# Optimization experiments

Hardware: AMD Instinct MI355X
Metric: run time of the kernel (lower is better)

The kernel has to match this reference:

```python
import jax, jax.numpy as jnp
import numpy as np

MARGIN = 0.2
LAMBDA_CLS = 1.0
LAMBDA_TRIPLET = 1.0
EPS = 1e-6  # matches torch pairwise_distance eps inside TripletMarginLoss
B, D, C = 8192, 192, 1024


def setup_inputs() -> dict:
    key = jax.random.key(0)
    k1, k2, k3 = jax.random.split(key, 3)
    embeddings = jax.random.normal(k1, (B, D), dtype=jnp.float32)
    logits = jax.random.normal(k2, (B, C), dtype=jnp.float32)
    targets = jax.random.randint(k3, (B,), 0, C, dtype=jnp.int64)
    return {"embeddings": embeddings, "logits": logits, "targets": targets}


def reference(embeddings, logits, targets):
    # ---- classification loss: mean cross entropy ----
    logp = jax.nn.log_softmax(logits, axis=-1)
    cls_loss = -jnp.mean(jnp.take_along_axis(logp, targets[:, None], axis=1))

    # ---- vectorized hard triplet mining (mining='hard'), on detached embeddings ----
    e = jax.lax.stop_gradient(embeddings)
    sq = jnp.sum(e * e, axis=1)                       # [B]
    d2 = sq[:, None] + sq[None, :] - 2.0 * (e @ e.T)  # [B, B]
    dist = jnp.sqrt(jnp.maximum(d2, 0.0))

    same = targets[:, None] == targets[None, :]       # [B, B]
    eye = jnp.eye(targets.shape[0], dtype=bool)
    pos_mask = same & ~eye
    neg_mask = ~same
    valid = pos_mask.any(axis=1) & neg_mask.any(axis=1)

    # hard positive: farthest same-speaker; hard negative: closest other-speaker
    pos_idx = jnp.argmax(jnp.where(pos_mask, dist, -jnp.inf), axis=1)
    neg_idx = jnp.argmin(jnp.where(neg_mask, dist, jnp.inf), axis=1)

    # ---- triplet margin loss on live embeddings ----
    a = embeddings
    p = embeddings[pos_idx]
    n = embeddings[neg_idx]
    d_ap = jnp.linalg.norm(a - p + EPS, axis=1)
    d_an = jnp.linalg.norm(a - n + EPS, axis=1)
    per_triplet = jnp.maximum(d_ap - d_an + MARGIN, 0.0)

    w = valid.astype(per_triplet.dtype)
    cnt = jnp.sum(w)
    trip_loss = jnp.where(cnt > 0, jnp.sum(per_triplet * w) / jnp.maximum(cnt, 1.0), 0.0)

    return LAMBDA_CLS * cls_loss + LAMBDA_TRIPLET * trip_loss
```

## Files before the change

### kernel.cpp

```cpp
#include <hip/hip_runtime.h>
#include <math.h>

#define B_N    8192
#define D_DIM  192
#define C_CLS  1024
#define MARGIN 0.2f
#define EPS_T  1e-6f

#define TI     128
#define TJ     128
#define JSPLIT 4
#define JLEN   (B_N / JSPLIT)
#define NT     (JLEN / TJ)
#define RB     384

typedef short v8s  __attribute__((ext_vector_type(8)));
typedef float v16f __attribute__((ext_vector_type(16)));

typedef __attribute__((address_space(3))) unsigned int       lds_u32;
typedef __attribute__((address_space(1))) const unsigned int glb_u32;

__device__ __forceinline__ void gll16(const void* g, void* l) {
  __builtin_amdgcn_global_load_lds((glb_u32*)g, (lds_u32*)l, 16, 0, 0);
}

__device__ __forceinline__ int swzb(int r, int cb) {
  return r * RB + (cb ^ ((r & 7) << 4));
}

__device__ __forceinline__ void stage_tile(char* dst, const char* src, int tid) {
  #pragma unroll
  for (int k = 0; k < 6; ++k) {
    int c  = k * 512 + tid;
    int r  = c / 24;
    int cb = (c - r * 24) * 16;
    gll16(src + r * RB + (cb ^ ((r & 7) << 4)),
          dst + (k * 512 + (tid & ~63)) * 16);
  }
}

__device__ __forceinline__ unsigned fkey(float f) {
  unsigned u = __float_as_uint(f);
  return (u & 0x80000000u) ? ~u : (u | 0x80000000u);
}

__device__ __forceinline__ unsigned short to_bf(float x) {
  unsigned u = __float_as_uint(x);
  u += 0x7fffu + ((u >> 16) & 1u);
  return (unsigned short)(u >> 16);
}

__global__ __launch_bounds__(256) void prep_kernel(
    const float* __restrict__ e, unsigned short* __restrict__ ebf,
    float* __restrict__ sq,
    unsigned long long* __restrict__ posw, unsigned long long* __restrict__ negw,
    float* __restrict__ accum) {
  int w = threadIdx.x >> 6, lane = threadIdx.x & 63;
  int row = blockIdx.x * 4 + w;
  const float* p = e + (size_t)row * D_DIM;
  float v0 = p[lane], v1 = p[lane + 64], v2 = p[lane + 128];
  unsigned short* q = ebf + (size_t)row * D_DIM;
  q[lane] = to_bf(v0); q[lane + 64] = to_bf(v1); q[lane + 128] = to_bf(v2);
  float s = v0 * v0 + v1 * v1 + v2 * v2;
  #pragma unroll
  for (int off = 32; off; off >>= 1) s += __shfl_xor(s, off);
  if (lane == 0) sq[row] = s;
  int b = blockIdx.x;
  if (b < 32)       posw[b * 256 + threadIdx.x] = 0ULL;
  else if (b < 64)  negw[(b - 32) * 256 + threadIdx.x] = ~0ULL;
  else if (b == 64 && threadIdx.x < 4) ((unsigned*)accum)[threadIdx.x] = 0u;
}

__global__ __launch_bounds__(512, 1) void mine_kernel(
    const unsigned short* __restrict__ ebf, const int* __restrict__ tgt,
    const float* __restrict__ sq, const float* __restrict__ logits,
    unsigned long long* __restrict__ posw, unsigned long long* __restrict__ negw,
    float* __restrict__ accum) {
  __shared__ unsigned short buf[2][TJ * (RB / 2)];
  __shared__ int   lds_t[2][TJ];
  __shared__ float lds_s[2][TJ];
  __shared__ unsigned long long pmrg[TI];
  __shared__ unsigned long long nmrg[TI];
  __shared__ float ce_part[8];

  const int tid  = threadIdx.x;
  const int w    = tid >> 6;
  const int lane = tid & 63;
  const int n5   = lane & 31;
  const int h    = lane >> 5;
  const int wj   = w & 3;
  const int wi   = w >> 2;
  const int i0 = blockIdx.x * TI;
  const int jb = blockIdx.y * JLEN;

  char* bufA = (char*)buf[0];
  char* bufB = (char*)buf[1];

  if (tid < TI) { pmrg[tid] = 0ULL; nmrg[tid] = ~0ULL; }

  stage_tile(bufB, (const char*)(ebf + (size_t)i0 * D_DIM), tid);
  stage_tile(bufA, (const char*)(ebf + (size_t)jb * D_DIM), tid);
  if (tid < TJ) { lds_t[0][tid] = tgt[jb + tid]; lds_s[0][tid] = sq[jb + tid]; }
  __syncthreads();

  v8s bfrag[2][12];
  #pragma unroll
  for (int tb = 0; tb < 2; ++tb)
    #pragma unroll
    for (int kc = 0; kc < 12; ++kc)
      bfrag[tb][kc] = *(const v8s*)(bufB + swzb(wi * 64 + tb * 32 + n5, kc * 32 + h * 16));

  int my_t[2];
  #pragma unroll
  for (int tb = 0; tb < 2; ++tb) my_t[tb] = tgt[i0 + wi * 64 + tb * 32 + n5];

  __syncthreads();

  float    pv[2] = {-3.4e38f, -3.4e38f}, nv[2] = {3.4e38f, 3.4e38f};
  unsigned pi_[2] = {0u, 0u}, ni_[2] = {0xFFFFFFFFu, 0xFFFFFFFFu};

  for (int t = 0; t < NT; ++t) {
    const int cur = t & 1;
    char* cbuf = (char*)buf[cur];

    if (t + 1 < NT) {
      int jn = jb + (t + 1) * TJ;
      stage_tile((char*)buf[cur ^ 1], (const char*)(ebf + (size_t)jn * D_DIM), tid);
      if (tid < TJ) { lds_t[cur ^ 1][tid] = tgt[jn + tid]; lds_s[cur ^ 1][tid] = sq[jn + tid]; }
    }

    v16f acc[2];
    #pragma unroll
    for (int tb = 0; tb < 2; ++tb)
      #pragma unroll
      for (int r = 0; r < 16; ++r) acc[tb][r] = 0.f;

    #pragma unroll
    for (int kc = 0; kc < 12; ++kc) {
      v8s afr = *(const v8s*)(cbuf + swzb(wj * 32 + n5, kc * 32 + h * 16));
      acc[0] = __builtin_amdgcn_mfma_f32_32x32x16_bf16(afr, bfrag[0][kc], acc[0], 0, 0, 0);
      acc[1] = __builtin_amdgcn_mfma_f32_32x32x16_bf16(afr, bfrag[1][kc], acc[1], 0, 0, 0);
    }

    const int j0 = jb + t * TJ;
    #pragma unroll
    for (int p = 0; p < 4; ++p) {
      int jb4 = wj * 32 + p * 8 + h * 4;
      float4 s4 = *(const float4*)&lds_s[cur][jb4];
      int4   t4 = *(const int4*)&lds_t[cur][jb4];
      #pragma unroll
      for (int q = 0; q < 4; ++q) {
        float sv = (q == 0) ? s4.x : (q == 1) ? s4.y : (q == 2) ? s4.z : s4.w;
        int   tv = (q == 0) ? t4.x : (q == 1) ? t4.y : (q == 2) ? t4.z : t4.w;
        unsigned jg = (unsigned)(j0 + jb4 + q);
        #pragma unroll
        for (int tb = 0; tb < 2; ++tb) {
          float val = fmaf(acc[tb][p * 4 + q], -2.0f, sv);
          bool same = (tv == my_t[tb]);
          float vp = same ? val : -3.4e38f;
          float vn = same ? 3.4e38f : val;
          if (vp > pv[tb]) { pv[tb] = vp; pi_[tb] = jg; }
          if (vn < nv[tb]) { nv[tb] = vn; ni_[tb] = jg; }
        }
      }
    }

    __syncthreads();
  }

  #pragma unroll
  for (int tb = 0; tb < 2; ++tb) {
    unsigned long long pk =
        ((unsigned long long)fkey(pv[tb]) << 32) | (unsigned long long)(unsigned)(~pi_[tb]);
    unsigned long long nk =
        ((unsigned long long)fkey(nv[tb]) << 32) | (unsigned long long)ni_[tb];
    unsigned long long po = __shfl_xor(pk, 32);
    unsigned long long no = __shfl_xor(nk, 32);
    pk = pk > po ? pk : po;
    nk = nk < no ? nk : no;
    if (h == 0) {
      atomicMax(&pmrg[wi * 64 + tb * 32 + n5], pk);
      atomicMin(&nmrg[wi * 64 + tb * 32 + n5], nk);
    }
  }
  __syncthreads();
  if (tid < TI) {
    atomicMax(&posw[i0 + tid], pmrg[tid]);
    atomicMin(&negw[i0 + tid], nmrg[tid]);
  }

  {
    int blin = blockIdx.y * 64 + blockIdx.x;
    float ce_acc = 0.f;
    #pragma unroll
    for (int it = 0; it < 4; ++it) {
      int row = blin * 32 + w * 4 + it;
      const float* lp = logits + (size_t)row * C_CLS;
      float4 x[4];
      #pragma unroll
      for (int u = 0; u < 4; ++u) x[u] = *(const float4*)(lp + lane * 4 + 256 * u);
      float m = -3.4e38f;
      #pragma unroll
      for (int u = 0; u < 4; ++u)
        m = fmaxf(m, fmaxf(fmaxf(x[u].x, x[u].y), fmaxf(x[u].z, x[u].w)));
      #pragma unroll
      for (int off = 32; off; off >>= 1) m = fmaxf(m, __shfl_xor(m, off));
      float s = 0.f;
      #pragma unroll
      for (int u = 0; u < 4; ++u)
        s += __expf(x[u].x - m) + __expf(x[u].y - m) +
             __expf(x[u].z - m) + __expf(x[u].w - m);
      #pragma unroll
      for (int off = 32; off; off >>= 1) s += __shfl_xor(s, off);
      if (lane == 0) ce_acc += m + __logf(s) - lp[tgt[row]];
    }
    if (lane == 0) ce_part[w] = ce_acc;
  }
  __syncthreads();
  if (tid == 0) {
    float a = 0.f;
    #pragma unroll
    for (int k = 0; k < 8; ++k) a += ce_part[k];
    atomicAdd(&accum[0], a);
  }
}

__global__ __launch_bounds__(1024) void trip_fin_kernel(
    const float* __restrict__ e,
    const unsigned long long* __restrict__ posw,
    const unsigned long long* __restrict__ negw,
    float* __restrict__ accum, float* __restrict__ out) {
  __shared__ float ssum[16];
  __shared__ float scnt[16];
  int w = threadIdx.x >> 6, lane = threadIdx.x & 63;
  int i = blockIdx.x * 16 + w;
  unsigned long long pp = posw[i], np = negw[i];
  unsigned pidx = ~(unsigned)pp;
  unsigned nidx = (unsigned)np;
  float res = 0.f, c = 0.f;
  if (pp != 0ULL && np != ~0ULL && pidx != (unsigned)i) {
    const float* pa = e + (size_t)i * D_DIM;
    const float* pb = e + (size_t)pidx * D_DIM;
    const float* pc = e + (size_t)nidx * D_DIM;
    float dap = 0.f, dan = 0.f;
    #pragma unroll
    for (int t = 0; t < 3; ++t) {
      int k = lane + 64 * t;
      float av = pa[k];
      float d1 = av - pb[k] + EPS_T;
      float d2 = av - pc[k] + EPS_T;
      dap += d1 * d1;
      dan += d2 * d2;
    }
    #pragma unroll
    for (int off = 32; off; off >>= 1) {
      dap += __shfl_xor(dap, off);
      dan += __shfl_xor(dan, off);
    }
    res = fmaxf(sqrtf(dap) - sqrtf(dan) + MARGIN, 0.f);
    c = 1.f;
  }
  if (lane == 0) { ssum[w] = res; scnt[w] = c; }
  __syncthreads();
  if (threadIdx.x == 0) {
    float a = 0.f, b = 0.f;
    #pragma unroll
    for (int k = 0; k < 16; ++k) { a += ssum[k]; b += scnt[k]; }
    atomicAdd(&accum[1], a);
    atomicAdd(&accum[2], b);
    __threadfence();
    unsigned old = atomicAdd((unsigned*)&accum[3], 1u);
    if (old == 511u) {
      __threadfence();
      float cls = atomicAdd(&accum[0], 0.f);
      float ts  = atomicAdd(&accum[1], 0.f);
      float tc  = atomicAdd(&accum[2], 0.f);
      float trip = (tc > 0.f) ? ts / fmaxf(tc, 1.f) : 0.f;
      out[0] = cls / (float)B_N + trip;
    }
  }
}

extern "C" void kernel_launch(void* const* d_in, const int* in_sizes, int n_in,
                              void* d_out, int out_size, void* d_ws, size_t ws_size,
                              hipStream_t stream) {
  const float* emb    = (const float*)d_in[0];
  const float* logits = (const float*)d_in[1];
  const int*   tgt    = (const int*)d_in[2];
  float* out = (float*)d_out;

  char* ws = (char*)d_ws;
  unsigned short* ebf = (unsigned short*)ws;
  unsigned long long* posw = (unsigned long long*)(ws + 3145728);
  unsigned long long* negw = (unsigned long long*)(ws + 3145728 + 65536);
  float* sq    = (float*)(ws + 3145728 + 131072);
  float* accum = (float*)(ws + 3145728 + 163840);

  prep_kernel<<<2048, 256, 0, stream>>>(emb, ebf, sq, posw, negw, accum);
  mine_kernel<<<dim3(B_N / TI, JSPLIT), 512, 0, stream>>>(ebf, tgt, sq, logits, posw, negw, accum);
  trip_fin_kernel<<<512, 1024, 0, stream>>>(emb, posw, negw, accum, out);
}
```

Baseline: 150.7 us.

## Preload all sq/targets to LDS and restructure tile prefetch with vmcnt waits

Loads the full JLEN slice of squared norms and targets into LDS once via global_load_lds, instead of staging 128 entries per tile. The j-tile prefetch is reorganised: the B-fragment buffer is reused for the second tile, and fine-grained s_waitcnt vmcnt counts plus raw s_barrier replace __syncthreads, so loads stay in flight across iterations. It also raises wave priority around the MFMA block and simplifies the argmax/argmin selects. The hand-counted vmcnt values are fragile and depend on how many loads stage_tile issues per thread.

Result: slower. 161.7 us (+7.3%).

```diff
diff --git a/kernel.cpp b/kernel.cpp
--- a/kernel.cpp
+++ b/kernel.cpp
@@ -77,8 +77,8 @@
     unsigned long long* __restrict__ posw, unsigned long long* __restrict__ negw,
     float* __restrict__ accum) {
   __shared__ unsigned short buf[2][TJ * (RB / 2)];
-  __shared__ int   lds_t[2][TJ];
-  __shared__ float lds_s[2][TJ];
+  __shared__ float lds_sq[JLEN];
+  __shared__ int   lds_tg[JLEN];
   __shared__ unsigned long long pmrg[TI];
   __shared__ unsigned long long nmrg[TI];
   __shared__ float ce_part[8];
@@ -98,10 +98,17 @@
 
   if (tid < TI) { pmrg[tid] = 0ULL; nmrg[tid] = ~0ULL; }
 
+  int my_t[2];
+  #pragma unroll
+  for (int tb = 0; tb < 2; ++tb) my_t[tb] = tgt[i0 + wi * 64 + tb * 32 + n5];
+
   stage_tile(bufB, (const char*)(ebf + (size_t)i0 * D_DIM), tid);
   stage_tile(bufA, (const char*)(ebf + (size_t)jb * D_DIM), tid);
-  if (tid < TJ) { lds_t[0][tid] = tgt[jb + tid]; lds_s[0][tid] = sq[jb + tid]; }
-  __syncthreads();
+  gll16((const char*)(sq  + jb) + tid * 16, (char*)lds_sq + (tid & ~63) * 16);
+  gll16((const char*)(tgt + jb) + tid * 16, (char*)lds_tg + (tid & ~63) * 16);
+  asm volatile("s_waitcnt vmcnt(8)" ::: "memory");
+  __builtin_amdgcn_s_barrier();
+  __builtin_amdgcn_sched_barrier(0);
 
   v8s bfrag[2][12];
   #pragma unroll
@@ -110,24 +117,21 @@
     for (int kc = 0; kc < 12; ++kc)
       bfrag[tb][kc] = *(const v8s*)(bufB + swzb(wi * 64 + tb * 32 + n5, kc * 32 + h * 16));
 
-  int my_t[2];
-  #pragma unroll
-  for (int tb = 0; tb < 2; ++tb) my_t[tb] = tgt[i0 + wi * 64 + tb * 32 + n5];
-
-  __syncthreads();
+  asm volatile("s_waitcnt lgkmcnt(0)" ::: "memory");
+  __builtin_amdgcn_s_barrier();
+
+  stage_tile(bufB, (const char*)(ebf + (size_t)(jb + TJ) * D_DIM), tid);
 
   float    pv[2] = {-3.4e38f, -3.4e38f}, nv[2] = {3.4e38f, 3.4e38f};
   unsigned pi_[2] = {0u, 0u}, ni_[2] = {0xFFFFFFFFu, 0xFFFFFFFFu};
 
   for (int t = 0; t < NT; ++t) {
-    const int cur = t & 1;
-    char* cbuf = (char*)buf[cur];
-
-    if (t + 1 < NT) {
-      int jn = jb + (t + 1) * TJ;
-      stage_tile((char*)buf[cur ^ 1], (const char*)(ebf + (size_t)jn * D_DIM), tid);
-      if (tid < TJ) { lds_t[cur ^ 1][tid] = tgt[jn + tid]; lds_s[cur ^ 1][tid] = sq[jn + tid]; }
-    }
+    char* cbuf = (t & 1) ? bufB : bufA;
+
+    if (t < NT - 1) asm volatile("s_waitcnt vmcnt(6)" ::: "memory");
+    else            asm volatile("s_waitcnt vmcnt(0)" ::: "memory");
+    __builtin_amdgcn_s_barrier();
+    __builtin_amdgcn_sched_barrier(0);
 
     v16f acc[2];
     #pragma unroll
@@ -135,19 +139,22 @@
       #pragma unroll
       for (int r = 0; r < 16; ++r) acc[tb][r] = 0.f;
 
+    __builtin_amdgcn_s_setprio(1);
     #pragma unroll
     for (int kc = 0; kc < 12; ++kc) {
       v8s afr = *(const v8s*)(cbuf + swzb(wj * 32 + n5, kc * 32 + h * 16));
       acc[0] = __builtin_amdgcn_mfma_f32_32x32x16_bf16(afr, bfrag[0][kc], acc[0], 0, 0, 0);
       acc[1] = __builtin_amdgcn_mfma_f32_32x32x16_bf16(afr, bfrag[1][kc], acc[1], 0, 0, 0);
     }
+    __builtin_amdgcn_s_setprio(0);
 
     const int j0 = jb + t * TJ;
+    const int jt = t * TJ;
     #pragma unroll
     for (int p = 0; p < 4; ++p) {
       int jb4 = wj * 32 + p * 8 + h * 4;
-      float4 s4 = *(const float4*)&lds_s[cur][jb4];
-      int4   t4 = *(const int4*)&lds_t[cur][jb4];
+      float4 s4 = *(const float4*)&lds_sq[jt + jb4];
+      int4   t4 = *(const int4*)&lds_tg[jt + jb4];
       #pragma unroll
       for (int q = 0; q < 4; ++q) {
         float sv = (q == 0) ? s4.x : (q == 1) ? s4.y : (q == 2) ? s4.z : s4.w;
@@ -157,16 +164,18 @@
         for (int tb = 0; tb < 2; ++tb) {
           float val = fmaf(acc[tb][p * 4 + q], -2.0f, sv);
           bool same = (tv == my_t[tb]);
-          float vp = same ? val : -3.4e38f;
-          float vn = same ? 3.4e38f : val;
-          if (vp > pv[tb]) { pv[tb] = vp; pi_[tb] = jg; }
-          if (vn < nv[tb]) { nv[tb] = vn; ni_[tb] = jg; }
+          if (same && val > pv[tb])  { pv[tb] = val; pi_[tb] = jg; }
+          if (!same && val < nv[tb]) { nv[tb] = val; ni_[tb] = jg; }
         }
       }
     }
 
-    __syncthreads();
-  }
+    __builtin_amdgcn_s_barrier();
+    if (t + 2 < NT)
+      stage_tile(cbuf, (const char*)(ebf + (size_t)(jb + (t + 2) * TJ) * D_DIM), tid);
+  }
+
+  __syncthreads();
 
   #pragma unroll
   for (int tb = 0; tb < 2; ++tb) {
```
